# Kernel optimization log

Hardware: AMD Instinct MI355X
Metric: run time of the kernel (lower is better)

The kernel has to match this reference:

```python
import jax, jax.numpy as jnp
import numpy as np

TEMPERATURE = 0.5
B, D = 4096, 256


def setup_inputs() -> dict:
    key = jax.random.key(0)
    k1, k2 = jax.random.split(key)
    emb_i = jax.random.normal(k1, (B, D), dtype=jnp.float32)
    emb_j = jax.random.normal(k2, (B, D), dtype=jnp.float32)
    return {"emb_i": emb_i, "emb_j": emb_j}


def reference(emb_i, emb_j):
    # NT-Xent (SimCLR) loss, vectorized version of the per-sample python loop.
    n = emb_i.shape[0]
    eps = 1e-12
    z_i = emb_i / jnp.maximum(jnp.linalg.norm(emb_i, axis=1, keepdims=True), eps)
    z_j = emb_j / jnp.maximum(jnp.linalg.norm(emb_j, axis=1, keepdims=True), eps)
    reps = jnp.concatenate([z_i, z_j], axis=0)               # [2N, D], unit rows
    # cosine similarity of unit vectors == dot product
    sim = reps @ reps.T                                       # [2N, 2N]
    exp_sim = jnp.exp(sim / TEMPERATURE)
    # denominator for row i: sum over k != i of exp(sim[i,k]/T)
    denom = jnp.sum(exp_sim, axis=1) - jnp.diagonal(exp_sim)  # [2N]
    # positive-pair sims: sim[k, k+N] and sim[k+N, k]
    pos = jnp.concatenate([jnp.diagonal(sim[:n, n:]), jnp.diagonal(sim[n:, :n])])
    # l_ij = log(exp(pos/T) / denom) = pos/T - log(denom)
    loss_terms = pos / TEMPERATURE - jnp.log(denom)
    return (1.0 / (2 * n)) * jnp.sum(loss_terms)
```

## Files before the change

kernel.cpp:

```cpp
#include <hip/hip_runtime.h>
#include <math.h>


#define NROWS 8192
#define NHALF 4096
#define DIM   256
#define BM    128
#define BN    128
#define NCB   (NROWS / BN)
#define NTRI  (NCB * (NCB + 1) / 2)

typedef __attribute__((ext_vector_type(8))) short bf16x8;
typedef __attribute__((ext_vector_type(4))) float f32x4;

static __device__ __forceinline__ unsigned short f2bf(float x) {
  unsigned int u = __float_as_uint(x);
  unsigned int r = (u + 0x7FFFu + ((u >> 16) & 1u)) >> 16;
  return (unsigned short)r;
}

__global__ __launch_bounds__(256) void normalize_kernel(
    const float* __restrict__ emb_i, const float* __restrict__ emb_j,
    unsigned short* __restrict__ zbF, float* __restrict__ out) {
  __shared__ unsigned short tile[16 * DIM];
  if (blockIdx.x == 0 && threadIdx.x == 0) out[0] = 0.f;
  const int w = threadIdx.x >> 6, lane = threadIdx.x & 63;
  const int rg = blockIdx.x;
  #pragma unroll
  for (int rr = 0; rr < 4; ++rr) {
    const int m16 = w * 4 + rr;
    const int row = rg * 16 + m16;
    const float* src = (row < NHALF) ? (emb_i + (size_t)row * DIM)
                                     : (emb_j + (size_t)(row - NHALF) * DIM);
    float4 v = ((const float4*)src)[lane];
    float ss = v.x * v.x + v.y * v.y + v.z * v.z + v.w * v.w;
    #pragma unroll
    for (int off = 32; off; off >>= 1) ss += __shfl_down(ss, off, 64);
    float total = __shfl(ss, 0, 64);
    float inv = 1.69870077f / fmaxf(sqrtf(total), 1e-12f);
    ushort4 o;
    o.x = f2bf(v.x * inv); o.y = f2bf(v.y * inv);
    o.z = f2bf(v.z * inv); o.w = f2bf(v.w * inv);
    const int ks = lane >> 3, quad = (lane >> 1) & 3, jj = (lane & 1) * 4;
    *(ushort4*)&tile[ks * 512 + (quad * 16 + m16) * 8 + jj] = o;
  }
  __syncthreads();
  uint4* dst = (uint4*)(zbF + (size_t)rg * (16 * DIM));
  const uint4* srcT = (const uint4*)tile;
  dst[threadIdx.x] = srcT[threadIdx.x];
  dst[256 + threadIdx.x] = srcT[256 + threadIdx.x];
}

__global__ __launch_bounds__(256, 4) void denom_kernel(
    const unsigned short* __restrict__ zbF, float* __restrict__ denomP,
    float* __restrict__ posv) {
  __shared__ unsigned short As[2][8 * 512];
  __shared__ unsigned short Bs[2][8 * 512];
  __shared__ float red[512];

  int t = (blockIdx.x & 7) * (NTRI / 8) + (blockIdx.x >> 3);
  int by = (int)((sqrtf(8.0f * (float)t + 1.0f) - 1.0f) * 0.5f);
  while ((by + 1) * (by + 2) / 2 <= t) ++by;
  while (by * (by + 1) / 2 > t) --by;
  int bx = t - by * (by + 1) / 2;

  const int tid = threadIdx.x;
  const int w = tid >> 6;
  const int lane = tid & 63;
  const int wr = w >> 1, wc = w & 1;
  const int quad = lane >> 4;
  const int m16 = lane & 15;
  const int row0 = bx * BM;
  const int col0 = by * BN;

  const unsigned short* gA = zbF + (size_t)(bx * 8) * 4096 + lane * 8;
  const unsigned short* gB = zbF + (size_t)(by * 8) * 4096 + lane * 8;

  f32x4 acc[4][4];
  #pragma unroll
  for (int i = 0; i < 4; ++i)
    #pragma unroll
    for (int j = 0; j < 4; ++j) {
      f32x4 z4 = {0.f, 0.f, 0.f, 0.f};
      acc[i][j] = z4;
    }

  auto stage = [&](int b, int ks) {
    #pragma unroll
    for (int r = 0; r < 2; ++r) {
      const int c = r * 4 + w;
      __builtin_amdgcn_global_load_lds(
          (const __attribute__((address_space(1))) unsigned int*)(gA +
              (size_t)c * 4096 + ks * 512),
          (__attribute__((address_space(3))) unsigned int*)&As[b][c * 512],
          16, 0, 0);
      __builtin_amdgcn_global_load_lds(
          (const __attribute__((address_space(1))) unsigned int*)(gB +
              (size_t)c * 4096 + ks * 512),
          (__attribute__((address_space(3))) unsigned int*)&Bs[b][c * 512],
          16, 0, 0);
    }
  };

  auto compute = [&](int b) {
    bf16x8 af[4], bfr[4];
    #pragma unroll
    for (int i = 0; i < 4; ++i)
      af[i] = *(const bf16x8*)&As[b][(wr * 4 + i) * 512 + lane * 8];
    #pragma unroll
    for (int j = 0; j < 4; ++j)
      bfr[j] = *(const bf16x8*)&Bs[b][(wc * 4 + j) * 512 + lane * 8];
    __builtin_amdgcn_s_setprio(1);
    #pragma unroll
    for (int i = 0; i < 4; ++i)
      #pragma unroll
      for (int j = 0; j < 4; ++j)
        acc[i][j] = __builtin_amdgcn_mfma_f32_16x16x32_bf16(
            af[i], bfr[j], acc[i][j], 0, 0, 0);
    __builtin_amdgcn_s_setprio(0);
  };

  stage(0, 0);
  __syncthreads();
  #pragma unroll
  for (int ks = 0; ks < 8; ++ks) {
    if (ks < 7) stage((ks + 1) & 1, ks + 1);
    compute(ks & 1);
    __syncthreads();
  }

  if (col0 - row0 == NHALF) {
    #pragma unroll
    for (int i = 0; i < 4; ++i)
      #pragma unroll
      for (int j = 0; j < 4; ++j) {
        int gcol = col0 + wc * 64 + j * 16 + m16;
        #pragma unroll
        for (int r = 0; r < 4; ++r) {
          int grow = row0 + wr * 64 + i * 16 + quad * 4 + r;
          if (gcol - grow == NHALF) posv[grow] = acc[i][j][r];
        }
      }
  }

  float rs[4][4];
  float cs[4] = {0.f, 0.f, 0.f, 0.f};
  #pragma unroll
  for (int i = 0; i < 4; ++i)
    #pragma unroll
    for (int r = 0; r < 4; ++r) rs[i][r] = 0.f;

  if (bx != by) {
    #pragma unroll
    for (int i = 0; i < 4; ++i)
      #pragma unroll
      for (int j = 0; j < 4; ++j)
        #pragma unroll
        for (int r = 0; r < 4; ++r) {
          float e = __builtin_amdgcn_exp2f(acc[i][j][r]);
          rs[i][r] += e;
          cs[j] += e;
        }
  } else {
    #pragma unroll
    for (int i = 0; i < 4; ++i)
      #pragma unroll
      for (int j = 0; j < 4; ++j) {
        int gcol = col0 + wc * 64 + j * 16 + m16;
        #pragma unroll
        for (int r = 0; r < 4; ++r) {
          int grow = row0 + wr * 64 + i * 16 + quad * 4 + r;
          float e =
              (grow == gcol) ? 0.f : __builtin_amdgcn_exp2f(acc[i][j][r]);
          rs[i][r] += e;
          cs[j] += e;
        }
      }
  }

  #pragma unroll
  for (int i = 0; i < 4; ++i)
    #pragma unroll
    for (int r = 0; r < 4; ++r) {
      float v = rs[i][r];
      v += __shfl_xor(v, 1, 16);
      v += __shfl_xor(v, 2, 16);
      v += __shfl_xor(v, 4, 16);
      v += __shfl_xor(v, 8, 16);
      if (m16 == 0) red[wc * 128 + wr * 64 + i * 16 + quad * 4 + r] = v;
    }
  #pragma unroll
  for (int j = 0; j < 4; ++j) {
    float v = cs[j];
    v += __shfl_xor(v, 16, 64);
    v += __shfl_xor(v, 32, 64);
    if (quad == 0) red[256 + wr * 128 + wc * 64 + j * 16 + m16] = v;
  }
  __syncthreads();

  if (tid < 128) {
    denomP[(size_t)by * NROWS + row0 + tid] = red[tid] + red[128 + tid];
  } else if (bx != by) {
    int c = tid - 128;
    denomP[(size_t)bx * NROWS + col0 + c] = red[256 + c] + red[384 + c];
  }
}

__global__ __launch_bounds__(256) void reduce_kernel(
    const float* __restrict__ denomP, const float* __restrict__ posv,
    float* __restrict__ out) {
  int tid = threadIdx.x;
  int r = blockIdx.x * 256 + tid;
  float s = 0.f;
  #pragma unroll 8
  for (int b = 0; b < NCB; ++b) s += denomP[(size_t)b * NROWS + r];
  float v = -logf(s);
  if (r < NHALF) v += 1.38629436112f * posv[r];
  #pragma unroll
  for (int off = 32; off; off >>= 1) v += __shfl_down(v, off, 64);
  __shared__ float s4[4];
  if ((tid & 63) == 0) s4[tid >> 6] = v;
  __syncthreads();
  if (tid == 0)
    atomicAdd(out, (s4[0] + s4[1] + s4[2] + s4[3]) * (1.0f / 8192.0f));
}

extern "C" void kernel_launch(void* const* d_in, const int* in_sizes, int n_in,
                              void* d_out, int out_size, void* d_ws,
                              size_t ws_size, hipStream_t stream) {
  const float* emb_i = (const float*)d_in[0];
  const float* emb_j = (const float*)d_in[1];
  unsigned short* zbF = (unsigned short*)d_ws;
  float* denomP = (float*)(zbF + (size_t)NROWS * DIM);
  float* posv = denomP + (size_t)NCB * NROWS;
  float* out = (float*)d_out;

  normalize_kernel<<<NROWS / 16, 256, 0, stream>>>(emb_i, emb_j, zbF, out);
  denom_kernel<<<NTRI, 256, 0, stream>>>(zbF, denomP, posv);
  reduce_kernel<<<NROWS / 256, 256, 0, stream>>>(denomP, posv, out);
}
```

Before: 94.55 us.

## Load B fragments directly to registers and fuse final reduction into GEMM kernel

The B operand is no longer staged through LDS. Each wave loads its B fragments straight from global memory into double-buffered registers, with explicit vmcnt waits and raw barriers in place of __syncthreads. The separate reduce kernel is removed: the last 32 blocks to finish, counted with an atomic ticket, wait until all blocks are done and then perform the row-sum, log and final accumulation. This cuts a kernel launch and halves LDS traffic and usage, at the cost of spin-waiting blocks and reliance on hand-tuned waitcnt ordering.

```diff
diff --git a/kernel.cpp b/kernel.cpp
--- a/kernel.cpp
+++ b/kernel.cpp
@@ -9,6 +9,7 @@
 #define BN    128
 #define NCB   (NROWS / BN)
 #define NTRI  (NCB * (NCB + 1) / 2)
+#define NRED  32
 
 typedef __attribute__((ext_vector_type(8))) short bf16x8;
 typedef __attribute__((ext_vector_type(4))) float f32x4;
@@ -21,9 +22,13 @@
 
 __global__ __launch_bounds__(256) void normalize_kernel(
     const float* __restrict__ emb_i, const float* __restrict__ emb_j,
-    unsigned short* __restrict__ zbF, float* __restrict__ out) {
+    unsigned short* __restrict__ zbF, float* __restrict__ out,
+    unsigned int* __restrict__ cnt) {
   __shared__ unsigned short tile[16 * DIM];
-  if (blockIdx.x == 0 && threadIdx.x == 0) out[0] = 0.f;
+  if (blockIdx.x == 0 && threadIdx.x == 0) {
+    out[0] = 0.f;
+    *cnt = 0u;
+  }
   const int w = threadIdx.x >> 6, lane = threadIdx.x & 63;
   const int rg = blockIdx.x;
   #pragma unroll
@@ -53,10 +58,11 @@
 
 __global__ __launch_bounds__(256, 4) void denom_kernel(
     const unsigned short* __restrict__ zbF, float* __restrict__ denomP,
-    float* __restrict__ posv) {
+    float* __restrict__ posv, float* __restrict__ out,
+    unsigned int* __restrict__ cnt) {
   __shared__ unsigned short As[2][8 * 512];
-  __shared__ unsigned short Bs[2][8 * 512];
   __shared__ float red[512];
+  __shared__ int tk;
 
   int t = (blockIdx.x & 7) * (NTRI / 8) + (blockIdx.x >> 3);
   int by = (int)((sqrtf(8.0f * (float)t + 1.0f) - 1.0f) * 0.5f);
@@ -74,7 +80,8 @@
   const int col0 = by * BN;
 
   const unsigned short* gA = zbF + (size_t)(bx * 8) * 4096 + lane * 8;
-  const unsigned short* gB = zbF + (size_t)(by * 8) * 4096 + lane * 8;
+  const unsigned short* gB =
+      zbF + (size_t)(by * 8 + wc * 4) * 4096 + lane * 8;
 
   f32x4 acc[4][4];
   #pragma unroll
@@ -85,7 +92,7 @@
       acc[i][j] = z4;
     }
 
-  auto stage = [&](int b, int ks) {
+  auto stageA = [&](int b, int ks) {
     #pragma unroll
     for (int r = 0; r < 2; ++r) {
       const int c = r * 4 + w;
@@ -94,40 +101,62 @@
               (size_t)c * 4096 + ks * 512),
           (__attribute__((address_space(3))) unsigned int*)&As[b][c * 512],
           16, 0, 0);
-      __builtin_amdgcn_global_load_lds(
-          (const __attribute__((address_space(1))) unsigned int*)(gB +
-              (size_t)c * 4096 + ks * 512),
-          (__attribute__((address_space(3))) unsigned int*)&Bs[b][c * 512],
-          16, 0, 0);
     }
   };
 
-  auto compute = [&](int b) {
-    bf16x8 af[4], bfr[4];
-    #pragma unroll
-    for (int i = 0; i < 4; ++i)
-      af[i] = *(const bf16x8*)&As[b][(wr * 4 + i) * 512 + lane * 8];
-    #pragma unroll
-    for (int j = 0; j < 4; ++j)
-      bfr[j] = *(const bf16x8*)&Bs[b][(wc * 4 + j) * 512 + lane * 8];
-    __builtin_amdgcn_s_setprio(1);
-    #pragma unroll
-    for (int i = 0; i < 4; ++i)
-      #pragma unroll
-      for (int j = 0; j < 4; ++j)
-        acc[i][j] = __builtin_amdgcn_mfma_f32_16x16x32_bf16(
-            af[i], bfr[j], acc[i][j], 0, 0, 0);
-    __builtin_amdgcn_s_setprio(0);
-  };
-
-  stage(0, 0);
-  __syncthreads();
-  #pragma unroll
-  for (int ks = 0; ks < 8; ++ks) {
-    if (ks < 7) stage((ks + 1) & 1, ks + 1);
-    compute(ks & 1);
-    __syncthreads();
-  }
+#define LOADB(BREG, ks)                                                    \
+  do {                                                                     \
+    _Pragma("unroll") for (int j = 0; j < 4; ++j)                          \
+        BREG[j] = *(const bf16x8*)(gB + (size_t)j * 4096 + (ks) * 512);    \
+  } while (0)
+
+#define COMPUTE(BUF, BREG)                                                 \
+  do {                                                                     \
+    _Pragma("unroll") for (int i = 0; i < 4; ++i) {                        \
+      bf16x8 af = *(const bf16x8*)&As[BUF][(wr * 4 + i) * 512 + lane * 8]; \
+      __builtin_amdgcn_s_setprio(1);                                       \
+      _Pragma("unroll") for (int j = 0; j < 4; ++j)                        \
+          acc[i][j] = __builtin_amdgcn_mfma_f32_16x16x32_bf16(             \
+              af, BREG[j], acc[i][j], 0, 0, 0);                            \
+      __builtin_amdgcn_s_setprio(0);                                       \
+    }                                                                      \
+  } while (0)
+
+  bf16x8 bE[4], bO[4];
+  stageA(0, 0);
+  LOADB(bE, 0);
+
+#define PHASE_PRE(ksp1, BUFN, BREGN)                                       \
+  do {                                                                     \
+    stageA(BUFN, ksp1);                                                    \
+    LOADB(BREGN, ksp1);                                                    \
+    asm volatile("s_waitcnt vmcnt(6)" ::: "memory");                       \
+  } while (0)
+#define PHASE_BODY(BUF, BREG)                                              \
+  do {                                                                     \
+    __builtin_amdgcn_s_barrier();                                          \
+    asm volatile("" ::: "memory");                                         \
+    COMPUTE(BUF, BREG);                                                    \
+    asm volatile("" ::: "memory");                                         \
+    __builtin_amdgcn_s_barrier();                                          \
+    asm volatile("" ::: "memory");                                         \
+  } while (0)
+
+  PHASE_PRE(1, 1, bO); PHASE_BODY(0, bE);
+  PHASE_PRE(2, 0, bE); PHASE_BODY(1, bO);
+  PHASE_PRE(3, 1, bO); PHASE_BODY(0, bE);
+  PHASE_PRE(4, 0, bE); PHASE_BODY(1, bO);
+  PHASE_PRE(5, 1, bO); PHASE_BODY(0, bE);
+  PHASE_PRE(6, 0, bE); PHASE_BODY(1, bO);
+  PHASE_PRE(7, 1, bO); PHASE_BODY(0, bE);
+  asm volatile("s_waitcnt vmcnt(0)" ::: "memory");
+  __builtin_amdgcn_s_barrier();
+  asm volatile("" ::: "memory");
+  COMPUTE(1, bO);
+#undef PHASE_PRE
+#undef PHASE_BODY
+#undef COMPUTE
+#undef LOADB
 
   if (col0 - row0 == NHALF) {
     #pragma unroll
@@ -204,13 +233,20 @@
     int c = tid - 128;
     denomP[(size_t)bx * NROWS + col0 + c] = red[256 + c] + red[384 + c];
   }
-}
-
-__global__ __launch_bounds__(256) void reduce_kernel(
-    const float* __restrict__ denomP, const float* __restrict__ posv,
-    float* __restrict__ out) {
-  int tid = threadIdx.x;
-  int r = blockIdx.x * 256 + tid;
+
+  __threadfence();
+  __syncthreads();
+  if (tid == 0) tk = (int)atomicAdd(cnt, 1u);
+  __syncthreads();
+  if (tk < NTRI - NRED) return;
+
+  if (tid == 0) {
+    while (atomicAdd(cnt, 0u) < (unsigned)NTRI) __builtin_amdgcn_s_sleep(8);
+  }
+  __syncthreads();
+  __threadfence();
+
+  const int r = (tk - (NTRI - NRED)) * 256 + tid;
   float s = 0.f;
   #pragma unroll 8
   for (int b = 0; b < NCB; ++b) s += denomP[(size_t)b * NROWS + r];
@@ -218,11 +254,11 @@
   if (r < NHALF) v += 1.38629436112f * posv[r];
   #pragma unroll
   for (int off = 32; off; off >>= 1) v += __shfl_down(v, off, 64);
-  __shared__ float s4[4];
-  if ((tid & 63) == 0) s4[tid >> 6] = v;
+  __syncthreads();
+  if ((tid & 63) == 0) red[tid >> 6] = v;
   __syncthreads();
   if (tid == 0)
-    atomicAdd(out, (s4[0] + s4[1] + s4[2] + s4[3]) * (1.0f / 8192.0f));
+    atomicAdd(out, (red[0] + red[1] + red[2] + red[3]) * (1.0f / 8192.0f));
 }
 
 extern "C" void kernel_launch(void* const* d_in, const int* in_sizes, int n_in,
@@ -233,9 +269,10 @@
   unsigned short* zbF = (unsigned short*)d_ws;
   float* denomP = (float*)(zbF + (size_t)NROWS * DIM);
   float* posv = denomP + (size_t)NCB * NROWS;
+  unsigned int* cnt = (unsigned int*)(posv + NHALF);
   float* out = (float*)d_out;
 
-  normalize_kernel<<<NROWS / 16, 256, 0, stream>>>(emb_i, emb_j, zbF, out);
-  denom_kernel<<<NTRI, 256, 0, stream>>>(zbF, denomP, posv);
-  reduce_kernel<<<NROWS / 256, 256, 0, stream>>>(denomP, posv, out);
-}
+  normalize_kernel<<<NROWS / 16, 256, 0, stream>>>(emb_i, emb_j, zbF, out,
+                                                   cnt);
+  denom_kernel<<<NTRI, 256, 0, stream>>>(zbF, denomP, posv, out, cnt);
+}
```

New measurement: 224.3 us. 2.37x slower.

## Enlarge symmetric-GEMM tiles to 256x256 with 512-thread blocks and explicit waitcnt pipeline

Applied to the files above, without the earlier changes.

Doubles the tile size of the triangular sim-matrix kernel from 128x128 to 256x256, using 8 waves per block each holding an 8x4 grid of MFMA accumulators, and stages K in 64-wide chunks across a 4-step double buffer. Barriers are placed by hand with vmcnt waits, replacing __syncthreads, so global-to-LDS loads overlap with compute. The goal is more reuse per loaded byte and fewer blocks. The cost is fewer blocks (528) on 256 CUs, larger LDS use and higher register pressure. The partial-denominator layout and the reduction stride are adjusted to match.

```diff
diff --git a/kernel.cpp b/kernel.cpp
--- a/kernel.cpp
+++ b/kernel.cpp
@@ -5,10 +5,10 @@
 #define NROWS 8192
 #define NHALF 4096
 #define DIM   256
-#define BM    128
-#define BN    128
-#define NCB   (NROWS / BN)
-#define NTRI  (NCB * (NCB + 1) / 2)
+#define BMT   256
+#define NCB   (NROWS / 128)
+#define NCBT  (NROWS / BMT)
+#define NTRIT (NCBT * (NCBT + 1) / 2)
 
 typedef __attribute__((ext_vector_type(8))) short bf16x8;
 typedef __attribute__((ext_vector_type(4))) float f32x4;
@@ -41,8 +41,8 @@
     ushort4 o;
     o.x = f2bf(v.x * inv); o.y = f2bf(v.y * inv);
     o.z = f2bf(v.z * inv); o.w = f2bf(v.w * inv);
-    const int ks = lane >> 3, quad = (lane >> 1) & 3, jj = (lane & 1) * 4;
-    *(ushort4*)&tile[ks * 512 + (quad * 16 + m16) * 8 + jj] = o;
+    const int s = lane >> 3, quad = (lane >> 1) & 3, jj = (lane & 1) * 4;
+    *(ushort4*)&tile[s * 512 + (quad * 16 + m16) * 8 + jj] = o;
   }
   __syncthreads();
   uint4* dst = (uint4*)(zbF + (size_t)rg * (16 * DIM));
@@ -51,14 +51,15 @@
   dst[256 + threadIdx.x] = srcT[256 + threadIdx.x];
 }
 
-__global__ __launch_bounds__(256, 4) void denom_kernel(
+__global__ __launch_bounds__(512, 2) void denom_kernel(
     const unsigned short* __restrict__ zbF, float* __restrict__ denomP,
     float* __restrict__ posv) {
-  __shared__ unsigned short As[2][8 * 512];
-  __shared__ unsigned short Bs[2][8 * 512];
-  __shared__ float red[512];
-
-  int t = (blockIdx.x & 7) * (NTRI / 8) + (blockIdx.x >> 3);
+  __shared__ unsigned short As[2][32 * 512];
+  __shared__ unsigned short Bs[2][32 * 512];
+  __shared__ float rowpart[4][256];
+  __shared__ float colpart[2][256];
+
+  int t = (blockIdx.x & 7) * (NTRIT / 8) + (blockIdx.x >> 3);
   int by = (int)((sqrtf(8.0f * (float)t + 1.0f) - 1.0f) * 0.5f);
   while ((by + 1) * (by + 2) / 2 <= t) ++by;
   while (by * (by + 1) / 2 > t) --by;
@@ -67,92 +68,114 @@
   const int tid = threadIdx.x;
   const int w = tid >> 6;
   const int lane = tid & 63;
-  const int wr = w >> 1, wc = w & 1;
+  const int wr = w >> 2, wc = w & 3;
   const int quad = lane >> 4;
   const int m16 = lane & 15;
-  const int row0 = bx * BM;
-  const int col0 = by * BN;
-
-  const unsigned short* gA = zbF + (size_t)(bx * 8) * 4096 + lane * 8;
-  const unsigned short* gB = zbF + (size_t)(by * 8) * 4096 + lane * 8;
-
-  f32x4 acc[4][4];
-  #pragma unroll
-  for (int i = 0; i < 4; ++i)
+  const int row0 = bx * BMT;
+  const int col0 = by * BMT;
+
+  const unsigned short* gA = zbF + (size_t)(bx * 16) * 4096 + lane * 8;
+  const unsigned short* gB = zbF + (size_t)(by * 16) * 4096 + lane * 8;
+
+  f32x4 acc[8][4];
+  #pragma unroll
+  for (int i = 0; i < 8; ++i)
     #pragma unroll
     for (int j = 0; j < 4; ++j) {
       f32x4 z4 = {0.f, 0.f, 0.f, 0.f};
       acc[i][j] = z4;
     }
 
-  auto stage = [&](int b, int ks) {
-    #pragma unroll
-    for (int r = 0; r < 2; ++r) {
-      const int c = r * 4 + w;
+  auto stage = [&](int b, int kt) {
+    #pragma unroll
+    for (int cc = 0; cc < 4; ++cc) {
+      const int c = w * 4 + cc;
+      const size_t goff = (size_t)(c >> 1) * 4096 + (kt * 2 + (c & 1)) * 512;
       __builtin_amdgcn_global_load_lds(
-          (const __attribute__((address_space(1))) unsigned int*)(gA +
-              (size_t)c * 4096 + ks * 512),
+          (const __attribute__((address_space(1))) unsigned int*)(gA + goff),
           (__attribute__((address_space(3))) unsigned int*)&As[b][c * 512],
           16, 0, 0);
       __builtin_amdgcn_global_load_lds(
-          (const __attribute__((address_space(1))) unsigned int*)(gB +
-              (size_t)c * 4096 + ks * 512),
+          (const __attribute__((address_space(1))) unsigned int*)(gB + goff),
           (__attribute__((address_space(3))) unsigned int*)&Bs[b][c * 512],
           16, 0, 0);
     }
   };
 
   auto compute = [&](int b) {
-    bf16x8 af[4], bfr[4];
-    #pragma unroll
-    for (int i = 0; i < 4; ++i)
-      af[i] = *(const bf16x8*)&As[b][(wr * 4 + i) * 512 + lane * 8];
-    #pragma unroll
-    for (int j = 0; j < 4; ++j)
-      bfr[j] = *(const bf16x8*)&Bs[b][(wc * 4 + j) * 512 + lane * 8];
-    __builtin_amdgcn_s_setprio(1);
-    #pragma unroll
-    for (int i = 0; i < 4; ++i)
+    #pragma unroll
+    for (int s32 = 0; s32 < 2; ++s32) {
+      bf16x8 af[8], bf[4];
+      #pragma unroll
+      for (int i = 0; i < 8; ++i)
+        af[i] = *(const bf16x8*)
+            &As[b][((wr * 8 + i) * 2 + s32) * 512 + lane * 8];
       #pragma unroll
       for (int j = 0; j < 4; ++j)
-        acc[i][j] = __builtin_amdgcn_mfma_f32_16x16x32_bf16(
-            af[i], bfr[j], acc[i][j], 0, 0, 0);
-    __builtin_amdgcn_s_setprio(0);
+        bf[j] = *(const bf16x8*)
+            &Bs[b][((wc * 4 + j) * 2 + s32) * 512 + lane * 8];
+      __builtin_amdgcn_s_setprio(1);
+      #pragma unroll
+      for (int i = 0; i < 8; ++i)
+        #pragma unroll
+        for (int j = 0; j < 4; ++j)
+          acc[i][j] = __builtin_amdgcn_mfma_f32_16x16x32_bf16(
+              af[i], bf[j], acc[i][j], 0, 0, 0);
+      __builtin_amdgcn_s_setprio(0);
+    }
   };
 
   stage(0, 0);
-  __syncthreads();
-  #pragma unroll
-  for (int ks = 0; ks < 8; ++ks) {
-    if (ks < 7) stage((ks + 1) & 1, ks + 1);
-    compute(ks & 1);
-    __syncthreads();
-  }
+  stage(1, 1);
+  asm volatile("s_waitcnt vmcnt(8)" ::: "memory");
+  __builtin_amdgcn_s_barrier();
+  asm volatile("" ::: "memory");
+  compute(0);
+  __builtin_amdgcn_s_barrier();
+  asm volatile("" ::: "memory");
+  stage(0, 2);
+  asm volatile("s_waitcnt vmcnt(8)" ::: "memory");
+  __builtin_amdgcn_s_barrier();
+  asm volatile("" ::: "memory");
+  compute(1);
+  __builtin_amdgcn_s_barrier();
+  asm volatile("" ::: "memory");
+  stage(1, 3);
+  asm volatile("s_waitcnt vmcnt(8)" ::: "memory");
+  __builtin_amdgcn_s_barrier();
+  asm volatile("" ::: "memory");
+  compute(0);
+  __builtin_amdgcn_s_barrier();
+  asm volatile("" ::: "memory");
+  asm volatile("s_waitcnt vmcnt(0)" ::: "memory");
+  __builtin_amdgcn_s_barrier();
+  asm volatile("" ::: "memory");
+  compute(1);
 
   if (col0 - row0 == NHALF) {
     #pragma unroll
-    for (int i = 0; i < 4; ++i)
+    for (int i = 0; i < 8; ++i)
       #pragma unroll
       for (int j = 0; j < 4; ++j) {
         int gcol = col0 + wc * 64 + j * 16 + m16;
         #pragma unroll
         for (int r = 0; r < 4; ++r) {
-          int grow = row0 + wr * 64 + i * 16 + quad * 4 + r;
+          int grow = row0 + wr * 128 + i * 16 + quad * 4 + r;
           if (gcol - grow == NHALF) posv[grow] = acc[i][j][r];
         }
       }
   }
 
-  float rs[4][4];
+  float rs[8][4];
   float cs[4] = {0.f, 0.f, 0.f, 0.f};
   #pragma unroll
-  for (int i = 0; i < 4; ++i)
+  for (int i = 0; i < 8; ++i)
     #pragma unroll
     for (int r = 0; r < 4; ++r) rs[i][r] = 0.f;
 
   if (bx != by) {
     #pragma unroll
-    for (int i = 0; i < 4; ++i)
+    for (int i = 0; i < 8; ++i)
       #pragma unroll
       for (int j = 0; j < 4; ++j)
         #pragma unroll
@@ -163,13 +186,13 @@
         }
   } else {
     #pragma unroll
-    for (int i = 0; i < 4; ++i)
+    for (int i = 0; i < 8; ++i)
       #pragma unroll
       for (int j = 0; j < 4; ++j) {
         int gcol = col0 + wc * 64 + j * 16 + m16;
         #pragma unroll
         for (int r = 0; r < 4; ++r) {
-          int grow = row0 + wr * 64 + i * 16 + quad * 4 + r;
+          int grow = row0 + wr * 128 + i * 16 + quad * 4 + r;
           float e =
               (grow == gcol) ? 0.f : __builtin_amdgcn_exp2f(acc[i][j][r]);
           rs[i][r] += e;
@@ -179,7 +202,7 @@
   }
 
   #pragma unroll
-  for (int i = 0; i < 4; ++i)
+  for (int i = 0; i < 8; ++i)
     #pragma unroll
     for (int r = 0; r < 4; ++r) {
       float v = rs[i][r];
@@ -187,22 +210,24 @@
       v += __shfl_xor(v, 2, 16);
       v += __shfl_xor(v, 4, 16);
       v += __shfl_xor(v, 8, 16);
-      if (m16 == 0) red[wc * 128 + wr * 64 + i * 16 + quad * 4 + r] = v;
+      if (m16 == 0) rowpart[wc][wr * 128 + i * 16 + quad * 4 + r] = v;
     }
   #pragma unroll
   for (int j = 0; j < 4; ++j) {
     float v = cs[j];
     v += __shfl_xor(v, 16, 64);
     v += __shfl_xor(v, 32, 64);
-    if (quad == 0) red[256 + wr * 128 + wc * 64 + j * 16 + m16] = v;
+    if (quad == 0) colpart[wr][wc * 64 + j * 16 + m16] = v;
   }
   __syncthreads();
 
-  if (tid < 128) {
-    denomP[(size_t)by * NROWS + row0 + tid] = red[tid] + red[128 + tid];
+  if (tid < 256) {
+    denomP[(size_t)(2 * by) * NROWS + row0 + tid] =
+        rowpart[0][tid] + rowpart[1][tid] + rowpart[2][tid] + rowpart[3][tid];
   } else if (bx != by) {
-    int c = tid - 128;
-    denomP[(size_t)bx * NROWS + col0 + c] = red[256 + c] + red[384 + c];
+    int c = tid - 256;
+    denomP[(size_t)(2 * bx) * NROWS + col0 + c] =
+        colpart[0][c] + colpart[1][c];
   }
 }
 
@@ -213,7 +238,7 @@
   int r = blockIdx.x * 256 + tid;
   float s = 0.f;
   #pragma unroll 8
-  for (int b = 0; b < NCB; ++b) s += denomP[(size_t)b * NROWS + r];
+  for (int b = 0; b < NCB; b += 2) s += denomP[(size_t)b * NROWS + r];
   float v = -logf(s);
   if (r < NHALF) v += 1.38629436112f * posv[r];
   #pragma unroll
@@ -236,6 +261,6 @@
   float* out = (float*)d_out;
 
   normalize_kernel<<<NROWS / 16, 256, 0, stream>>>(emb_i, emb_j, zbF, out);
-  denom_kernel<<<NTRI, 256, 0, stream>>>(zbF, denomP, posv);
+  denom_kernel<<<NTRIT, 512, 0, stream>>>(zbF, denomP, posv);
   reduce_kernel<<<NROWS / 256, 256, 0, stream>>>(denomP, posv, out);
 }
```

After: 106.6 us. 12.8% more time.
